# Optimization experiments

Measured on AMD Instinct MI355X. Metric: run time of the kernel, lower is better.

The kernel has to match this reference:

```python
import jax, jax.numpy as jnp
import numpy as np

STD = np.array([0.1, 0.1, 0.2, 0.2], dtype=np.float32)  # RPN_bounding_box_std_dev
PRE_NMS_LIMIT = 6000
PROPOSAL_COUNT = 1000
NMS_THRESHOLD = 0.7


def setup_inputs() -> dict:
    key = jax.random.key(0)
    k1, k2, k3, k4 = jax.random.split(key, 4)
    B, N = 4, 262144
    scores = jax.random.uniform(k1, (B, N, 2), dtype=jnp.float32)
    deltas = jax.random.normal(k2, (B, N, 4), dtype=jnp.float32)
    # valid normalized anchors (x_min, y_min, x_max, y_max) in [0,1]
    centers = jax.random.uniform(k3, (B, N, 2), dtype=jnp.float32)
    sizes = jax.random.uniform(k4, (B, N, 2), dtype=jnp.float32) * 0.28 + 0.02
    mins = jnp.clip(centers - 0.5 * sizes, 0.0, 1.0)
    maxs = jnp.clip(centers + 0.5 * sizes, 0.0, 1.0)
    anchors = jnp.concatenate([mins, maxs], axis=-1)
    return {"scores": scores, "deltas": deltas, "anchors": anchors}


def apply_box_delta(boxes, deltas):
    # boxes: [..., (x_min, y_min, x_max, y_max)]; deltas: [..., (dx, dy, log dw, log dh)]
    w = boxes[..., 2] - boxes[..., 0]
    h = boxes[..., 3] - boxes[..., 1]
    cx = boxes[..., 0] + 0.5 * w
    cy = boxes[..., 1] + 0.5 * h
    cx = cx + deltas[..., 0] * w
    cy = cy + deltas[..., 1] * h
    w = w * jnp.exp(deltas[..., 2])
    h = h * jnp.exp(deltas[..., 3])
    return jnp.stack([cx - 0.5 * w, cy - 0.5 * h, cx + 0.5 * w, cy + 0.5 * h], axis=-1)


def _iou_matrix(b):
    # b: [N, 4] -> [N, N]
    area = (b[:, 2] - b[:, 0]) * (b[:, 3] - b[:, 1])
    lt = jnp.maximum(b[:, None, :2], b[None, :, :2])
    rb = jnp.minimum(b[:, None, 2:], b[None, :, 2:])
    wh = jnp.clip(rb - lt, 0.0)
    inter = wh[..., 0] * wh[..., 1]
    return inter / (area[:, None] + area[None, :] - inter + 1e-12)


def _nms_pad(boxes, thr, count):
    # boxes sorted by descending score; greedy NMS, gather kept, pad to `count`.
    n = boxes.shape[0]
    iou = _iou_matrix(boxes)
    order = jnp.arange(n)

    def step(keep, i):
        suppress = keep[i] & (iou[i] > thr) & (order > i)
        return keep & ~suppress, None

    keep, _ = jax.lax.scan(step, jnp.ones((n,), dtype=bool), order)
    rank = jnp.cumsum(keep.astype(jnp.int32)) - 1
    valid = keep & (rank < count)
    idx = jnp.where(valid, rank, count)  # invalid rows scatter into scratch row
    out = jnp.zeros((count + 1, 4), boxes.dtype)
    out = out.at[idx].set(jnp.where(valid[:, None], boxes, 0.0))
    return out[:count]


def reference(scores, deltas, anchors):
    fg_scores = scores[:, :, 1]                                   # [B, N]
    deltas = deltas * jnp.asarray(STD).reshape(1, 1, 4)
    k = min(PRE_NMS_LIMIT, anchors.shape[1])
    top_scores, idx = jax.lax.top_k(fg_scores, k)                 # sorted desc
    top_deltas = jnp.take_along_axis(deltas, idx[..., None], axis=1)
    top_anchors = jnp.take_along_axis(anchors, idx[..., None], axis=1)
    boxes = apply_box_delta(top_anchors, top_deltas)
    boxes = jnp.clip(boxes, 0.0, 1.0)                             # window [0,0,1,1]
    proposals = jax.vmap(lambda b: _nms_pad(b, NMS_THRESHOLD, PROPOSAL_COUNT))(boxes)
    return proposals  # [B, proposal_count, 4]
```

## Files before the change

### kernel.cpp

```cpp
#include <hip/hip_runtime.h>
#include <stdint.h>

#define NB 4
#define NN 262144
#define KTOP 6000
#define NPROP 1000
#define MAXCAND 8192
#define MROWS 2048
#define NWORDS 32
#define BOXSTRIDE 6016
#define NCHUNK 64
#define NBLK (NB*NCHUNK)

#define GH_OFF    0
#define THR_OFF   131072
#define CNT_OFF   131136
#define KEYS_OFF  131584
#define BOX_OFF   (KEYS_OFF + NB*MAXCAND*8)
#define MASK_OFF  (BOX_OFF + NB*BOXSTRIDE*16)

__global__ __launch_bounds__(256) void k1_hist(const float* __restrict__ scores,
                                               int* __restrict__ ghist_pb) {
  __shared__ int lh[128];
  int blk = blockIdx.x, b = blk >> 6, chunk = blk & 63;
  if (threadIdx.x < 128) lh[threadIdx.x] = 0;
  __syncthreads();
  const float* sc = scores + (((size_t)b * NN + (size_t)chunk * 4096) * 2);
  for (int it = 0; it < 16; ++it) {
    unsigned int bits = __float_as_uint(sc[(it * 256 + threadIdx.x) * 2 + 1]);
    if (bits >= 0x3F000000u && bits < 0x80000000u) {
      int bk = (int)((bits >> 16) - 0x3F00u); if (bk > 127) bk = 127;
      atomicAdd(&lh[bk], 1);
    }
  }
  __syncthreads();
  if (threadIdx.x < 128) ghist_pb[blk * 128 + threadIdx.x] = lh[threadIdx.x];
}

__global__ __launch_bounds__(128) void k2_thresh(const int* __restrict__ gh,
                                                 int* __restrict__ thr, int* __restrict__ cnt) {
  __shared__ int h[128];
  int b = blockIdx.x, t = threadIdx.x;
  int s = 0;
  for (int c = 0; c < NCHUNK; ++c) s += gh[((b << 6) + c) * 128 + t];
  h[t] = s;
  __syncthreads();
  if (t == 0) {
    int acc = 0, th = 0;
    for (int bk = 127; bk >= 0; --bk) { acc += h[bk]; if (acc >= KTOP) { th = bk; break; } }
    thr[b] = th;
    cnt[b * 16] = 0;
  }
}

__global__ __launch_bounds__(256) void k3_compact(const float* __restrict__ scores,
                                                  const int* __restrict__ thr,
                                                  int* __restrict__ cnt,
                                                  unsigned long long* __restrict__ keys) {
  int blk = blockIdx.x, b = blk >> 6, chunk = blk & 63;
  int tid = threadIdx.x, lane = tid & 63, w = tid >> 6;
  const float* sc = scores + (((size_t)b * NN + (size_t)chunk * 4096) * 2);
  unsigned int thrbits = (0x3F00u + (unsigned int)thr[b]) << 16;
  unsigned long long below = (lane == 0) ? 0ULL : ((~0ULL) >> (64 - lane));
  __shared__ int woff[4];
  unsigned int bitsArr[16];
  int wcount = 0;
  for (int it = 0; it < 16; ++it) {
    unsigned int bits = __float_as_uint(sc[(it * 256 + tid) * 2 + 1]);
    bitsArr[it] = bits;
    bool pass = (bits < 0x80000000u) && (bits >= thrbits);
    wcount += (int)__popcll(__ballot(pass));
  }
  if (lane == 0) woff[w] = wcount;
  __syncthreads();
  if (tid == 0) {
    int t0 = woff[0], t1 = woff[1], t2 = woff[2], t3 = woff[3];
    int base = atomicAdd(&cnt[b * 16], t0 + t1 + t2 + t3);
    woff[0] = base; woff[1] = base + t0; woff[2] = base + t0 + t1; woff[3] = base + t0 + t1 + t2;
  }
  __syncthreads();
  int running = woff[w];
  for (int it = 0; it < 16; ++it) {
    unsigned int bits = bitsArr[it];
    bool pass = (bits < 0x80000000u) && (bits >= thrbits);
    unsigned long long act = __ballot(pass);
    if (pass) {
      int pos = running + (int)__popcll(act & below);
      if (pos < MAXCAND) {
        unsigned int n = (unsigned int)(chunk * 4096 + it * 256 + tid);
        keys[(b << 13) + pos] = ((unsigned long long)bits << 32) | (unsigned long long)(0xFFFFFFFFu - n);
      }
    }
    running += (int)__popcll(act);
  }
}

__global__ __launch_bounds__(1024) void k4_sort(const int* __restrict__ cnt,
                                                const unsigned long long* __restrict__ keys,
                                                const int* __restrict__ thr,
                                                int* __restrict__ sidx) {
  __shared__ unsigned int skeys[MAXCAND];
  __shared__ int cntb[4096];
  __shared__ int offb[4096];
  int b = blockIdx.x;
  int tid = threadIdx.x;
  int c = cnt[b * 16]; if (c > MAXCAND) c = MAXCAND;
  unsigned int thrbits = (0x3F00u + (unsigned int)thr[b]) << 16;
  unsigned int R = 0x3F800000u - thrbits;
  int bitlen = 32 - __clz((int)R);
  int shift = (bitlen > 12) ? (bitlen - 12) : 0;
  unsigned int lowmask = (shift > 0) ? ((1u << shift) - 1u) : 0u;
  for (int i = tid; i < 4096; i += 1024) cntb[i] = 0;
  __syncthreads();
  int bin8[8]; unsigned int pay8[8];
  #pragma unroll
  for (int i = 0; i < 8; ++i) {
    int t = i * 1024 + tid;
    bin8[i] = -1;
    if (t < c) {
      unsigned long long key = keys[(b << 13) + t];
      unsigned int sbits = (unsigned int)(key >> 32);
      unsigned int nidx  = (unsigned int)key & 0x3FFFFu;
      unsigned int rel = sbits - thrbits;
      int bin = (int)(rel >> shift);
      bin8[i] = bin;
      pay8[i] = ((rel & lowmask) << 18) | nidx;
      atomicAdd(&cntb[bin], 1);
    }
  }
  __syncthreads();
  unsigned int* temp = skeys;
  int lc0 = cntb[4095 - 4 * tid], lc1 = cntb[4094 - 4 * tid],
      lc2 = cntb[4093 - 4 * tid], lc3 = cntb[4092 - 4 * tid];
  int tsum = lc0 + lc1 + lc2 + lc3;
  int v = tsum;
  temp[tid] = (unsigned int)v;
  __syncthreads();
  for (int d = 1; d < 1024; d <<= 1) {
    int add = (tid >= d) ? (int)temp[tid - d] : 0;
    __syncthreads();
    v += add;
    temp[tid] = (unsigned int)v;
    __syncthreads();
  }
  int excl = v - tsum;
  offb[4095 - 4 * tid] = excl;
  offb[4094 - 4 * tid] = excl + lc0;
  offb[4093 - 4 * tid] = excl + lc0 + lc1;
  offb[4092 - 4 * tid] = excl + lc0 + lc1 + lc2;
  __syncthreads();
  #pragma unroll
  for (int i = 0; i < 8; ++i) {
    if (bin8[i] >= 0) {
      int pos = atomicAdd(&offb[bin8[i]], 1);
      skeys[pos] = pay8[i];
    }
  }
  __syncthreads();
  #pragma unroll
  for (int k = 0; k < 4; ++k) {
    int h = 4 * tid + k;
    int n = cntb[h];
    if (n > 1) {
      int base = offb[h] - n;
      for (int i = 0; i < n - 1; ++i) {
        int mx = i; unsigned int mv = skeys[base + i];
        for (int j = i + 1; j < n; ++j) {
          unsigned int vv = skeys[base + j];
          if (vv > mv) { mv = vv; mx = j; }
        }
        if (mx != i) { skeys[base + mx] = skeys[base + i]; skeys[base + i] = mv; }
      }
    }
  }
  __syncthreads();
  for (int t = tid; t < KTOP; t += 1024) {
    int src = (t < c) ? (int)(0x3FFFFu - (skeys[t] & 0x3FFFFu)) : -1;
    sidx[(b << 14) + t] = src;
  }
}

__global__ __launch_bounds__(256) void k5_boxes(const float* __restrict__ deltas,
                                                const float* __restrict__ anchors,
                                                const int* __restrict__ sidx,
                                                float4* __restrict__ boxes) {
  int b = blockIdx.y;
  int cand = blockIdx.x * 256 + threadIdx.x;
  if (cand >= KTOP) return;
  int src = sidx[(b << 14) + cand];
  float4 r = make_float4(0.f, 0.f, 0.f, 0.f);
  if (src >= 0) {
    const float4* anc4 = (const float4*)anchors;
    const float4* del4 = (const float4*)deltas;
    float4 a = anc4[(size_t)b * NN + src];
    float4 d = del4[(size_t)b * NN + src];
    float d0 = d.x * 0.1f, d1 = d.y * 0.1f, d2 = d.z * 0.2f, d3 = d.w * 0.2f;
    float w = a.z - a.x, h = a.w - a.y;
    float cx = a.x + 0.5f * w, cy = a.y + 0.5f * h;
    cx += d0 * w; cy += d1 * h;
    w *= expf(d2); h *= expf(d3);
    r.x = fminf(fmaxf(cx - 0.5f * w, 0.f), 1.f);
    r.y = fminf(fmaxf(cy - 0.5f * h, 0.f), 1.f);
    r.z = fminf(fmaxf(cx + 0.5f * w, 0.f), 1.f);
    r.w = fminf(fmaxf(cy + 0.5f * h, 0.f), 1.f);
  }
  boxes[b * BOXSTRIDE + cand] = r;
}

__global__ __launch_bounds__(256) void k6_mask(const float4* __restrict__ boxes,
                                               unsigned long long* __restrict__ mask) {
  int b = blockIdx.y;
  int r0 = blockIdx.x * 64;
  __shared__ float4 rb[64];
  __shared__ float4 cb[256];
  int tid = threadIdx.x;
  if (tid < 64) rb[tid] = boxes[b * BOXSTRIDE + r0 + tid];
  __syncthreads();
  int row = tid >> 2, w = tid & 3;
  float4 R = rb[row];
  float ar = (R.z - R.x) * (R.w - R.y);
  for (int jt = 0; jt < MROWS / 256; ++jt) {
    cb[tid] = boxes[b * BOXSTRIDE + jt * 256 + tid];
    __syncthreads();
    unsigned long long bits = 0ULL;
    int cbase = w * 64;
    #pragma unroll 8
    for (int k = 0; k < 64; ++k) {
      float4 C = cb[cbase + k];
      float ac = (C.z - C.x) * (C.w - C.y);
      float lx = fmaxf(R.x, C.x), ly = fmaxf(R.y, C.y);
      float hx = fminf(R.z, C.z), hy = fminf(R.w, C.w);
      float iw = fmaxf(hx - lx, 0.f), ih = fmaxf(hy - ly, 0.f);
      float inter = iw * ih;
      if (inter > 0.7f * (ar + ac - inter + 1e-12f)) bits |= (1ULL << k);
    }
    mask[((size_t)(b * MROWS + r0 + row) << 5) + (size_t)(jt * 4 + w)] = bits;
    __syncthreads();
  }
}

__global__ __launch_bounds__(64) void k7_scan(const unsigned long long* __restrict__ mask,
                                              const float4* __restrict__ boxes,
                                              float4* __restrict__ out) {
  int b = blockIdx.x;
  int lane = threadIdx.x;
  __shared__ float4 kbox[NPROP];
  const unsigned long long* M = mask + ((size_t)b * MROWS * NWORDS);
  const float4* BX = boxes + b * BOXSTRIDE;
  unsigned long long below = (lane == 0) ? 0ULL : ((~0ULL) >> (64 - lane));
  int half = lane >> 5;
  int wsel = lane & 31;
  unsigned long long supp = 0ULL;
  int kept = 0;
  for (int c = 0; c < MROWS / 64 && kept < NPROP; ++c) {
    int base = c * 64;
    unsigned long long diag = M[(size_t)(base + lane) * NWORDS + c];
    float4 mybox = BX[base + lane];
    unsigned long long mrow[32];
    #pragma unroll
    for (int i = 0; i < 32; ++i)
      mrow[i] = M[(size_t)(base + 2 * i + half) * NWORDS + wsel];
    unsigned int slo = (unsigned int)supp, shi = (unsigned int)(supp >> 32);
    unsigned long long suppc =
        ((unsigned long long)(unsigned int)(__builtin_amdgcn_readlane(shi, c) |
                                            __builtin_amdgcn_readlane(shi, c + 32)) << 32) |
        (unsigned long long)(unsigned int)(__builtin_amdgcn_readlane(slo, c) |
                                           __builtin_amdgcn_readlane(slo, c + 32));
    unsigned int dlo = (unsigned int)diag, dhi = (unsigned int)(diag >> 32);
    unsigned long long keeprows = 0ULL;
    #pragma unroll
    for (int k = 0; k < 64; ++k) {
      unsigned long long dk =
          ((unsigned long long)(unsigned int)__builtin_amdgcn_readlane(dhi, k) << 32) |
          (unsigned long long)(unsigned int)__builtin_amdgcn_readlane(dlo, k);
      if (((suppc >> k) & 1ULL) == 0ULL) { keeprows |= (1ULL << k); suppc |= dk; }
    }
    bool mykeep = ((keeprows >> lane) & 1ULL) != 0ULL;
    int pos = kept + (int)__popcll(keeprows & below);
    if (mykeep && pos < NPROP) { out[b * NPROP + pos] = mybox; kbox[pos] = mybox; }
    #pragma unroll
    for (int i = 0; i < 32; ++i) {
      int r = 2 * i + half;
      if ((keeprows >> r) & 1ULL) supp |= mrow[i];
    }
    kept += (int)__popcll(keeprows);
  }
  if (kept > NPROP) kept = NPROP;
  __syncthreads();
  for (int cc = MROWS; cc < KTOP && kept < NPROP; ++cc) {
    float4 C = BX[cc];
    float ac = (C.z - C.x) * (C.w - C.y);
    bool over = false;
    for (int j = lane; j < kept; j += 64) {
      float4 K = kbox[j];
      float ak = (K.z - K.x) * (K.w - K.y);
      float lx = fmaxf(C.x, K.x), ly = fmaxf(C.y, K.y);
      float hx = fminf(C.z, K.z), hy = fminf(C.w, K.w);
      float iw = fmaxf(hx - lx, 0.f), ih = fmaxf(hy - ly, 0.f);
      float inter = iw * ih;
      if (inter > 0.7f * (ac + ak - inter + 1e-12f)) over = true;
    }
    if (__ballot(over) == 0ULL) {
      if (lane == 0) { out[b * NPROP + kept] = C; kbox[kept] = C; }
      kept++;
    }
    __syncthreads();
  }
  for (int r = kept + lane; r < NPROP; r += 64) out[b * NPROP + r] = make_float4(0.f, 0.f, 0.f, 0.f);
}

extern "C" void kernel_launch(void* const* d_in, const int* in_sizes, int n_in,
                              void* d_out, int out_size, void* d_ws, size_t ws_size,
                              hipStream_t stream) {
  const float* scores  = (const float*)d_in[0];
  const float* deltas  = (const float*)d_in[1];
  const float* anchors = (const float*)d_in[2];
  char* ws = (char*)d_ws;
  int* gh   = (int*)(ws + GH_OFF);
  int* thr  = (int*)(ws + THR_OFF);
  int* cnt  = (int*)(ws + CNT_OFF);
  unsigned long long* keys = (unsigned long long*)(ws + KEYS_OFF);
  int* sidx = (int*)(ws + KEYS_OFF);
  float4* boxes = (float4*)(ws + BOX_OFF);
  unsigned long long* mask = (unsigned long long*)(ws + MASK_OFF);
  float4* out = (float4*)d_out;

  hipLaunchKernelGGL(k1_hist,   dim3(NBLK), dim3(256),  0, stream, scores, gh);
  hipLaunchKernelGGL(k2_thresh, dim3(NB),   dim3(128),  0, stream, gh, thr, cnt);
  hipLaunchKernelGGL(k3_compact,dim3(NBLK), dim3(256),  0, stream, scores, thr, cnt, keys);
  hipLaunchKernelGGL(k4_sort,   dim3(NB),   dim3(1024), 0, stream, cnt, keys, thr, sidx);
  hipLaunchKernelGGL(k5_boxes,  dim3((KTOP + 255) / 256, NB), dim3(256), 0, stream, deltas, anchors, sidx, boxes);
  hipLaunchKernelGGL(k6_mask,   dim3(MROWS / 64, NB), dim3(256), 0, stream, boxes, mask);
  hipLaunchKernelGGL(k7_scan,   dim3(NB),   dim3(64),   0, stream, mask, boxes, out);
}
```

Before: 181.1 us.

## Split NMS mask scan across four waves with prefetched mask rows

The serial NMS scan kernel now runs with 256 threads instead of one wave. Wave 0 resolves each 64-row chunk's diagonal, while all threads OR the kept rows' mask words into an LDS suppression vector using atomics. Each thread holds 8 mask words instead of 32, and the next chunk's rows, diagonal and boxes are loaded one iteration ahead so load latency overlaps the serial resolve. The cost is two block barriers and LDS atomics per chunk, and only the upper-triangular words (w > c) are loaded.

```diff
diff --git a/kernel.cpp b/kernel.cpp
--- a/kernel.cpp
+++ b/kernel.cpp
@@ -239,74 +239,102 @@
   }
 }
 
-__global__ __launch_bounds__(64) void k7_scan(const unsigned long long* __restrict__ mask,
-                                              const float4* __restrict__ boxes,
-                                              float4* __restrict__ out) {
+__global__ __launch_bounds__(256) void k7_scan(const unsigned long long* __restrict__ mask,
+                                               const float4* __restrict__ boxes,
+                                               float4* __restrict__ out) {
   int b = blockIdx.x;
-  int lane = threadIdx.x;
+  int tid = threadIdx.x;
+  int wave = tid >> 6, lane = tid & 63;
+  int w = tid & 31;
+  int g = tid >> 5;
   __shared__ float4 kbox[NPROP];
+  __shared__ unsigned long long lds_supp[NWORDS];
+  __shared__ unsigned long long lds_keepw;
+  __shared__ int lds_kept;
   const unsigned long long* M = mask + ((size_t)b * MROWS * NWORDS);
   const float4* BX = boxes + b * BOXSTRIDE;
   unsigned long long below = (lane == 0) ? 0ULL : ((~0ULL) >> (64 - lane));
-  int half = lane >> 5;
-  int wsel = lane & 31;
-  unsigned long long supp = 0ULL;
+
+  if (tid < NWORDS) lds_supp[tid] = 0ULL;
+  if (tid == 0) lds_kept = 0;
+  unsigned long long psupp = 0ULL;
+  int keptw0 = 0;
+
+  unsigned long long mrow[8];
+  unsigned long long diag = 0ULL;
+  float4 mybox = make_float4(0.f, 0.f, 0.f, 0.f);
+  #pragma unroll
+  for (int i = 0; i < 8; ++i)
+    mrow[i] = (w > 0) ? M[(size_t)(g + 8 * i) * NWORDS + w] : 0ULL;
+  if (wave == 0) { diag = M[(size_t)lane * NWORDS]; mybox = BX[lane]; }
+  __syncthreads();
+
   int kept = 0;
-  for (int c = 0; c < MROWS / 64 && kept < NPROP; ++c) {
-    int base = c * 64;
-    unsigned long long diag = M[(size_t)(base + lane) * NWORDS + c];
-    float4 mybox = BX[base + lane];
-    unsigned long long mrow[32];
+  for (int c = 0; c < MROWS / 64; ++c) {
+    unsigned long long mrow_n[8] = {0ULL,0ULL,0ULL,0ULL,0ULL,0ULL,0ULL,0ULL};
+    unsigned long long diag_n = 0ULL;
+    float4 mybox_n = make_float4(0.f, 0.f, 0.f, 0.f);
+    if (c + 1 < MROWS / 64) {
+      int nb = (c + 1) * 64;
+      #pragma unroll
+      for (int i = 0; i < 8; ++i)
+        if (w > c + 1) mrow_n[i] = M[(size_t)(nb + g + 8 * i) * NWORDS + w];
+      if (wave == 0) { diag_n = M[(size_t)(nb + lane) * NWORDS + (c + 1)]; mybox_n = BX[nb + lane]; }
+    }
+    if (wave == 0) {
+      unsigned long long suppc = lds_supp[c];
+      unsigned int dlo = (unsigned int)diag, dhi = (unsigned int)(diag >> 32);
+      unsigned long long keeprows = 0ULL;
+      #pragma unroll
+      for (int k = 0; k < 64; ++k) {
+        unsigned long long dk =
+            ((unsigned long long)(unsigned int)__builtin_amdgcn_readlane(dhi, k) << 32) |
+            (unsigned long long)(unsigned int)__builtin_amdgcn_readlane(dlo, k);
+        if (((suppc >> k) & 1ULL) == 0ULL) { keeprows |= (1ULL << k); suppc |= dk; }
+      }
+      bool mykeep = ((keeprows >> lane) & 1ULL) != 0ULL;
+      int pos = keptw0 + (int)__popcll(keeprows & below);
+      if (mykeep && pos < NPROP) { out[b * NPROP + pos] = mybox; kbox[pos] = mybox; }
+      keptw0 += (int)__popcll(keeprows);
+      if (lane == 0) { lds_keepw = keeprows; lds_kept = keptw0; }
+    }
+    __syncthreads();
+    unsigned long long keeprows = lds_keepw;
+    kept = lds_kept;
     #pragma unroll
-    for (int i = 0; i < 32; ++i)
-      mrow[i] = M[(size_t)(base + 2 * i + half) * NWORDS + wsel];
-    unsigned int slo = (unsigned int)supp, shi = (unsigned int)(supp >> 32);
-    unsigned long long suppc =
-        ((unsigned long long)(unsigned int)(__builtin_amdgcn_readlane(shi, c) |
-                                            __builtin_amdgcn_readlane(shi, c + 32)) << 32) |
-        (unsigned long long)(unsigned int)(__builtin_amdgcn_readlane(slo, c) |
-                                           __builtin_amdgcn_readlane(slo, c + 32));
-    unsigned int dlo = (unsigned int)diag, dhi = (unsigned int)(diag >> 32);
-    unsigned long long keeprows = 0ULL;
+    for (int i = 0; i < 8; ++i)
+      if ((keeprows >> (g + 8 * i)) & 1ULL) psupp |= mrow[i];
+    if (w > c) atomicOr(&lds_supp[w], psupp);
     #pragma unroll
-    for (int k = 0; k < 64; ++k) {
-      unsigned long long dk =
-          ((unsigned long long)(unsigned int)__builtin_amdgcn_readlane(dhi, k) << 32) |
-          (unsigned long long)(unsigned int)__builtin_amdgcn_readlane(dlo, k);
-      if (((suppc >> k) & 1ULL) == 0ULL) { keeprows |= (1ULL << k); suppc |= dk; }
-    }
-    bool mykeep = ((keeprows >> lane) & 1ULL) != 0ULL;
-    int pos = kept + (int)__popcll(keeprows & below);
-    if (mykeep && pos < NPROP) { out[b * NPROP + pos] = mybox; kbox[pos] = mybox; }
-    #pragma unroll
-    for (int i = 0; i < 32; ++i) {
-      int r = 2 * i + half;
-      if ((keeprows >> r) & 1ULL) supp |= mrow[i];
-    }
-    kept += (int)__popcll(keeprows);
-  }
-  if (kept > NPROP) kept = NPROP;
-  __syncthreads();
-  for (int cc = MROWS; cc < KTOP && kept < NPROP; ++cc) {
-    float4 C = BX[cc];
-    float ac = (C.z - C.x) * (C.w - C.y);
-    bool over = false;
-    for (int j = lane; j < kept; j += 64) {
-      float4 K = kbox[j];
-      float ak = (K.z - K.x) * (K.w - K.y);
-      float lx = fmaxf(C.x, K.x), ly = fmaxf(C.y, K.y);
-      float hx = fminf(C.z, K.z), hy = fminf(C.w, K.w);
-      float iw = fmaxf(hx - lx, 0.f), ih = fmaxf(hy - ly, 0.f);
-      float inter = iw * ih;
-      if (inter > 0.7f * (ac + ak - inter + 1e-12f)) over = true;
-    }
-    if (__ballot(over) == 0ULL) {
-      if (lane == 0) { out[b * NPROP + kept] = C; kbox[kept] = C; }
-      kept++;
-    }
-    __syncthreads();
-  }
-  for (int r = kept + lane; r < NPROP; r += 64) out[b * NPROP + r] = make_float4(0.f, 0.f, 0.f, 0.f);
+    for (int i = 0; i < 8; ++i) mrow[i] = mrow_n[i];
+    diag = diag_n; mybox = mybox_n;
+    if (kept >= NPROP) break;
+    __syncthreads();
+  }
+
+  if (wave == 0) {
+    int k2 = (keptw0 > NPROP) ? NPROP : keptw0;
+    for (int cc = MROWS; cc < KTOP && k2 < NPROP; ++cc) {
+      float4 C = BX[cc];
+      float ac = (C.z - C.x) * (C.w - C.y);
+      bool over = false;
+      for (int j = lane; j < k2; j += 64) {
+        float4 K = kbox[j];
+        float ak = (K.z - K.x) * (K.w - K.y);
+        float lx = fmaxf(C.x, K.x), ly = fmaxf(C.y, K.y);
+        float hx = fminf(C.z, K.z), hy = fminf(C.w, K.w);
+        float iw = fmaxf(hx - lx, 0.f), ih = fmaxf(hy - ly, 0.f);
+        float inter = iw * ih;
+        if (inter > 0.7f * (ac + ak - inter + 1e-12f)) over = true;
+      }
+      if (__ballot(over) == 0ULL) {
+        if (lane == 0) { out[b * NPROP + k2] = C; kbox[k2] = C; }
+        k2++;
+      }
+    }
+    for (int r = k2 + lane; r < NPROP; r += 64)
+      out[b * NPROP + r] = make_float4(0.f, 0.f, 0.f, 0.f);
+  }
 }
 
 extern "C" void kernel_launch(void* const* d_in, const int* in_sizes, int n_in,
@@ -331,5 +359,5 @@
   hipLaunchKernelGGL(k4_sort,   dim3(NB),   dim3(1024), 0, stream, cnt, keys, thr, sidx);
   hipLaunchKernelGGL(k5_boxes,  dim3((KTOP + 255) / 256, NB), dim3(256), 0, stream, deltas, anchors, sidx, boxes);
   hipLaunchKernelGGL(k6_mask,   dim3(MROWS / 64, NB), dim3(256), 0, stream, boxes, mask);
-  hipLaunchKernelGGL(k7_scan,   dim3(NB),   dim3(64),   0, stream, mask, boxes, out);
-}
+  hipLaunchKernelGGL(k7_scan,   dim3(NB),   dim3(256), 0, stream, mask, boxes, out);
+}
```

New measurement: 184.6 us. About the same (+1.9%).
